# Kernel tuning notes

Hardware: AMD Instinct MI355X
Metric: run time of the kernel (lower is better)

## Reference

```python
import jax, jax.numpy as jnp
import numpy as np

N_ATOMS = 50000   # nAtoms
KMAX = 32         # max neighbors per atom
EMB_ATOM = 256    # emb_size_atom
EMB_PAIR_IN = 64  # emb_size_pair_in
EMB_PAIR_OUT = 64 # emb_size_pair_out
EMB_RBF = 16      # emb_size_rbf
INV_SQRT = lambda n: 1.0 / np.sqrt(n).astype(np.float32)


def setup_inputs() -> dict:
    key = jax.random.key(0)
    k_h, k_rb, k_src, k_wd, k_wb, k_wu = jax.random.split(key, 6)
    h = jax.random.normal(k_h, (N_ATOMS, EMB_ATOM), dtype=jnp.float32)
    rad_basis = jax.random.normal(k_rb, (N_ATOMS, EMB_RBF, KMAX), dtype=jnp.float32)
    # each destination atom has exactly KMAX neighbors -> unique (dst, slot) pairs
    dst = jnp.repeat(jnp.arange(N_ATOMS, dtype=jnp.int64), KMAX)
    src = jax.random.randint(k_src, (N_ATOMS * KMAX,), 0, N_ATOMS, dtype=jnp.int64)
    edge_index = jnp.stack([src, dst])  # (2, nEdges)
    target_neighbor_idx = jnp.tile(jnp.arange(KMAX, dtype=jnp.int64), N_ATOMS)
    W_down = jax.random.normal(k_wd, (EMB_ATOM, EMB_PAIR_IN), dtype=jnp.float32) * INV_SQRT(EMB_ATOM)
    W_bilinear = jax.random.normal(k_wb, (EMB_RBF * EMB_PAIR_IN, EMB_PAIR_OUT), dtype=jnp.float32) * INV_SQRT(EMB_RBF * EMB_PAIR_IN)
    W_up = jax.random.normal(k_wu, (EMB_PAIR_OUT, EMB_ATOM), dtype=jnp.float32) * INV_SQRT(EMB_PAIR_OUT)
    return {"h": h, "rad_basis": rad_basis, "edge_index": edge_index,
            "target_neighbor_idx": target_neighbor_idx,
            "W_down": W_down, "W_bilinear": W_bilinear, "W_up": W_up}


def reference(h, rad_basis, edge_index, target_neighbor_idx, W_down, W_bilinear, W_up):
    num_atoms = h.shape[0]
    kmax = rad_basis.shape[-1]
    # down projection (no bias, no activation)
    x_b = h @ W_down                               # (nAtoms, emb_pair_in)
    x_ba = x_b[edge_index[0]]                      # (nEdges, emb_pair_in) gather from source atoms
    # scatter into dense padded tensor (nAtoms, Kmax, emb_pair_in)
    x2 = jnp.zeros((num_atoms, kmax, x_ba.shape[-1]), dtype=x_ba.dtype)
    x2 = x2.at[edge_index[1], target_neighbor_idx].set(x_ba)
    # per-atom batched matmul with radial basis: (nAtoms, emb_rbf, Kmax) @ (nAtoms, Kmax, emb_pair_in)
    x_ba2 = jnp.einsum('nrk,nkp->nrp', rad_basis, x2)
    # bilinear projection on flattened (emb_rbf * emb_pair_in); ScaleFactor default scale = 1.0 (identity)
    h_out = x_ba2.reshape(num_atoms, -1) @ W_bilinear  # (nAtoms, emb_pair_out)
    return h_out @ W_up                               # (nAtoms, emb_size_atom)
```

## Files before the change

kernel.cpp:

```cpp
#include <hip/hip_runtime.h>

#define N_ATOMS 50000
#define KMAX 32
#define EMB_ATOM 256
#define EP_IN 64
#define EP_OUT 64
#define EMB_RBF 16
#define NEDGES (N_ATOMS * KMAX)

typedef _Float16 half_t;
typedef __attribute__((ext_vector_type(2))) _Float16 half2_t;
typedef __attribute__((ext_vector_type(4))) _Float16 half4_t;
typedef __attribute__((ext_vector_type(8))) _Float16 half8_t;
typedef __attribute__((ext_vector_type(4))) float f32x4;

static_assert(N_ATOMS % 16 == 0, "fused kernel assumes 16 atoms per block");

#define GLOAD_LDS16(g, l)                                                     \
    __builtin_amdgcn_global_load_lds(                                         \
        (const __attribute__((address_space(1))) void*)(g),                   \
        (__attribute__((address_space(3))) void*)(l), 16, 0, 0)

#define XB_NB 782
#define SC_NB (NEDGES / 256)
#define WB_NB 256
#define WU_NB 64
#define PREP_NB (XB_NB + SC_NB + WB_NB + WU_NB + 1)

__global__ __launch_bounds__(256) void prep_all(const float* __restrict__ h,
                                                const float* __restrict__ Wd,
                                                const int*   __restrict__ ei,
                                                const int*   __restrict__ tni,
                                                const float* __restrict__ Wb,
                                                const float* __restrict__ Wu,
                                                half_t* __restrict__ xbh,
                                                int*    __restrict__ sidx,
                                                half_t* __restrict__ Wb2,
                                                half_t* __restrict__ Wu2,
                                                half_t* __restrict__ zrow) {
    __shared__ float As[16 * 68];
    __shared__ float Bs[16 * 64];
    const int bid = blockIdx.x;
    const int t = threadIdx.x;

    if (bid < XB_NB) {
        const int r0 = bid * 64;
        const int tr = t >> 4, tc = t & 15;
        float acc[4][4] = {};
        for (int k0 = 0; k0 < 256; k0 += 16) {
            {
                int m = t >> 2, kk0 = (t & 3) << 2;
                int row = r0 + m;
                float4 v = make_float4(0.f, 0.f, 0.f, 0.f);
                if (row < N_ATOMS)
                    v = *reinterpret_cast<const float4*>(&h[(size_t)row * 256 + k0 + kk0]);
                As[(kk0 + 0) * 68 + m] = v.x;
                As[(kk0 + 1) * 68 + m] = v.y;
                As[(kk0 + 2) * 68 + m] = v.z;
                As[(kk0 + 3) * 68 + m] = v.w;
            }
            {
                int kk = t >> 4, n0 = (t & 15) << 2;
                *reinterpret_cast<float4*>(&Bs[kk * 64 + n0]) =
                    *reinterpret_cast<const float4*>(&Wd[(k0 + kk) * 64 + n0]);
            }
            __syncthreads();
            #pragma unroll
            for (int kk = 0; kk < 16; ++kk) {
                float4 av = *reinterpret_cast<const float4*>(&As[kk * 68 + tr * 4]);
                float4 bv = *reinterpret_cast<const float4*>(&Bs[kk * 64 + tc * 4]);
                float aa[4] = {av.x, av.y, av.z, av.w};
                float bb[4] = {bv.x, bv.y, bv.z, bv.w};
                #pragma unroll
                for (int i = 0; i < 4; ++i)
                    #pragma unroll
                    for (int j = 0; j < 4; ++j) acc[i][j] += aa[i] * bb[j];
            }
            __syncthreads();
        }
        #pragma unroll
        for (int i = 0; i < 4; ++i) {
            int row = r0 + tr * 4 + i;
            if (row < N_ATOMS) {
                half4_t hv;
                #pragma unroll
                for (int j = 0; j < 4; ++j) hv[j] = (half_t)acc[i][j];
                *reinterpret_cast<half4_t*>(&xbh[(size_t)row * 64 + tc * 4]) = hv;
            }
        }
    } else if (bid < XB_NB + SC_NB) {
        int i = (bid - XB_NB) * 256 + t;
        int s = ei[i];
        int d = ei[NEDGES + i];
        int k = tni[i];
        sidx[d * KMAX + k] = s;
    } else if (bid < XB_NB + SC_NB + WB_NB) {
        int i = (bid - XB_NB - SC_NB) * 256 + t;
        int e = i & 7, lv = (i >> 3) & 63;
        int c = lv & 15, g = lv >> 4;
        int kh = (i >> 13) & 1, ot = i >> 14;
        int o = ot * 16 + c;
        int idx = kh * 512 + ((i >> 9) & 15) * 32 + g * 8 + e;
        int r = ((idx >> 6) & 3) * 4 + (idx & 3);
        int p = (idx >> 8) * 16 + ((idx >> 2) & 15);
        Wb2[i] = (half_t)Wb[(size_t)(r * 64 + p) * 64 + o];
    } else if (bid < XB_NB + SC_NB + WB_NB + WU_NB) {
        int i = (bid - XB_NB - SC_NB - WB_NB) * 256 + t;
        int e = i & 7, lv = (i >> 3) & 63;
        int c = lv & 15, g = lv >> 4;
        int kk = (i >> 9) & 1, nt = (i >> 10) & 1, w = i >> 11;
        int oc = w * 32 + nt * 16 + c;
        int o = kk * 32 + g * 8 + e;
        Wu2[i] = (half_t)Wu[(size_t)o * 256 + oc];
    } else {
        if (t < 128) zrow[t] = (half_t)0.f;
    }
}

template <int BUF>
__device__ __forceinline__ void consume_batch(const half_t* stage_h, int c, int g,
                                              half4_t radf, half4_t ident,
                                              f32x4 (&acc)[4]) {
    const f32x4 fzero = {0.f, 0.f, 0.f, 0.f};
    const char* stb = reinterpret_cast<const char*>(stage_h) + BUF * 2048;
    #pragma unroll
    for (int pc = 0; pc < 4; ++pc) {
        int slot = (pc * 2 + (g >> 1)) ^ (c & 7);
        half4_t gf = *reinterpret_cast<const half4_t*>(
            stb + c * 128 + slot * 16 + (g & 1) * 8);
        f32x4 tD = __builtin_amdgcn_mfma_f32_16x16x16f16(gf, ident, fzero, 0, 0, 0);
        half4_t b2;
        #pragma unroll
        for (int j = 0; j < 4; ++j) b2[j] = (half_t)tD[j];
        acc[pc] = __builtin_amdgcn_mfma_f32_16x16x16f16(radf, b2, acc[pc], 0, 0, 0);
    }
}

#define ISSUE(b, buf) do {                                                    \
    { int s_ = sreg[(b) * 2 + 0]; int r_ = (l >> 3);                          \
      const half_t* src_ = ((unsigned)s_ < (unsigned)N_ATOMS)                 \
          ? (xbh + (size_t)s_ * 64) : zrow;                                   \
      src_ += (((l & 7) ^ (r_ & 7)) << 3);                                    \
      GLOAD_LDS16(src_, stage_h + (buf) * 1024); }                            \
    { int s_ = sreg[(b) * 2 + 1]; int r_ = 8 + (l >> 3);                      \
      const half_t* src_ = ((unsigned)s_ < (unsigned)N_ATOMS)                 \
          ? (xbh + (size_t)s_ * 64) : zrow;                                   \
      src_ += (((l & 7) ^ (r_ & 7)) << 3);                                    \
      GLOAD_LDS16(src_, stage_h + (buf) * 1024 + 512); }                      \
} while (0)

#define WAIT_VM(n) do {                                                       \
    asm volatile("s_waitcnt vmcnt(" #n ")" ::: "memory");                     \
    __builtin_amdgcn_sched_barrier(0);                                        \
} while (0)

#define WAIT_LGKM() do {                                                      \
    asm volatile("s_waitcnt lgkmcnt(0)" ::: "memory");                        \
    __builtin_amdgcn_sched_barrier(0);                                        \
} while (0)

__global__ __launch_bounds__(512, 4) void fused(const half_t* __restrict__ xbh,
                                                const float*  __restrict__ rad,
                                                const int*    __restrict__ sidxg,
                                                const half_t* __restrict__ Wb2,
                                                const half_t* __restrict__ Wu2,
                                                const half_t* __restrict__ zrow,
                                                float* __restrict__ out) {
    __shared__ __align__(16) half_t xba2s[16 * 1024];
    __shared__ __align__(16) char   smem_u[32768];

    const int t = threadIdx.x;
    const int w = t >> 6;
    const int l = t & 63;
    const int c = l & 15;
    const int g = l >> 4;
    const int a0 = blockIdx.x * 16;

    float*  preds   = reinterpret_cast<float*>(smem_u);
    half_t* houts   = reinterpret_cast<half_t*>(smem_u + 8704);
    half_t* stage_h = reinterpret_cast<half_t*>(smem_u + (w << 12));

    const f32x4 fzero = {0.f, 0.f, 0.f, 0.f};

    int sreg[4 * 2];
    #pragma unroll
    for (int b = 0; b < 4; ++b)
        #pragma unroll
        for (int hh = 0; hh < 2; ++hh)
            sreg[b * 2 + hh] = sidxg[(size_t)(a0 + w * 2 + (b >> 1)) * KMAX +
                                     (b & 1) * 16 + hh * 8 + (l >> 3)];

    half4_t radF[2][2];
    #pragma unroll
    for (int as = 0; as < 2; ++as) {
        const float* radp = &rad[(size_t)(a0 + w * 2 + as) * 512];
        #pragma unroll
        for (int kc = 0; kc < 2; ++kc) {
            f32x4 rv = *reinterpret_cast<const f32x4*>(radp + c * 32 + kc * 16 + g * 4);
            #pragma unroll
            for (int j = 0; j < 4; ++j) radF[as][kc][j] = (half_t)rv[j];
        }
    }

    half4_t ident;
    #pragma unroll
    for (int j = 0; j < 4; ++j) ident[j] = (half_t)((g * 4 + j == c) ? 1.0f : 0.0f);

    ISSUE(0, 0);
    ISSUE(1, 1);

    f32x4 acc[4] = {fzero, fzero, fzero, fzero};

    WAIT_VM(2);
    consume_batch<0>(stage_h, c, g, radF[0][0], ident, acc);
    WAIT_LGKM();
    ISSUE(2, 0);

    WAIT_VM(2);
    consume_batch<1>(stage_h, c, g, radF[0][1], ident, acc);
    {
        const int a = w * 2;
        #pragma unroll
        for (int pc = 0; pc < 4; ++pc) {
            half4_t hv;
            #pragma unroll
            for (int j = 0; j < 4; ++j) hv[j] = (half_t)acc[pc][j];
            int byte = (a * 2048 + pc * 512 + g * 128 + c * 8) ^ ((a & 7) << 4);
            *reinterpret_cast<half4_t*>(reinterpret_cast<char*>(xba2s) + byte) = hv;
        }
    }
    WAIT_LGKM();
    ISSUE(3, 1);

    #pragma unroll
    for (int pc = 0; pc < 4; ++pc) acc[pc] = fzero;

    WAIT_VM(2);
    consume_batch<0>(stage_h, c, g, radF[1][0], ident, acc);

    WAIT_VM(0);
    consume_batch<1>(stage_h, c, g, radF[1][1], ident, acc);
    {
        const int a = w * 2 + 1;
        #pragma unroll
        for (int pc = 0; pc < 4; ++pc) {
            half4_t hv;
            #pragma unroll
            for (int j = 0; j < 4; ++j) hv[j] = (half_t)acc[pc][j];
            int byte = (a * 2048 + pc * 512 + g * 128 + c * 8) ^ ((a & 7) << 4);
            *reinterpret_cast<half4_t*>(reinterpret_cast<char*>(xba2s) + byte) = hv;
        }
    }

    const int ot = w >> 1, kh = w & 1;
    const half_t* wbbase = &Wb2[(size_t)((ot * 2 + kh) * 16) * 512];
    half8_t bfr[4];
    #pragma unroll
    for (int j = 0; j < 4; ++j)
        bfr[j] = *reinterpret_cast<const half8_t*>(wbbase + j * 512 + l * 8);

    __syncthreads();

    {
        f32x4 acc2[4] = {fzero, fzero, fzero, fzero};
        #pragma unroll
        for (int j = 0; j < 16; ++j) {
            int abyte = (c * 2048 + (kh * 512 + j * 32) * 2 + g * 16) ^ ((c & 7) << 4);
            half8_t af = *reinterpret_cast<const half8_t*>(
                reinterpret_cast<const char*>(xba2s) + abyte);
            half8_t bf = bfr[j & 3];
            if (j + 4 < 16)
                bfr[j & 3] = *reinterpret_cast<const half8_t*>(wbbase + (j + 4) * 512 + l * 8);
            acc2[j & 3] = __builtin_amdgcn_mfma_f32_16x16x32_f16(af, bf, acc2[j & 3], 0, 0, 0);
        }
        f32x4 accT = acc2[0] + acc2[1] + acc2[2] + acc2[3];
        #pragma unroll
        for (int i = 0; i < 4; ++i)
            preds[kh * 1088 + (g * 4 + i) * 68 + ot * 16 + c] = accT[i];
    }

    half8_t wuf[2][2];
    #pragma unroll
    for (int nt = 0; nt < 2; ++nt)
        #pragma unroll
        for (int kk = 0; kk < 2; ++kk)
            wuf[nt][kk] = *reinterpret_cast<const half8_t*>(
                &Wu2[(size_t)(((w * 2 + nt) * 2 + kk) * 64 + l) * 8]);

    __syncthreads();

    {
        int m = t >> 5, oj = (t & 31) << 1;
        float s0 = preds[m * 68 + oj]     + preds[1088 + m * 68 + oj];
        float s1 = preds[m * 68 + oj + 1] + preds[1088 + m * 68 + oj + 1];
        half2_t hv; hv[0] = (half_t)s0; hv[1] = (half_t)s1;
        int byte = (m * 128 + oj * 2) ^ ((m & 7) << 4);
        *reinterpret_cast<half2_t*>(reinterpret_cast<char*>(houts) + byte) = hv;
    }
    __syncthreads();

    half8_t ha[2];
    #pragma unroll
    for (int kk = 0; kk < 2; ++kk) {
        int byte = (c * 128 + kk * 64 + g * 16) ^ ((c & 7) << 4);
        ha[kk] = *reinterpret_cast<const half8_t*>(
            reinterpret_cast<const char*>(houts) + byte);
    }
    #pragma unroll
    for (int nt = 0; nt < 2; ++nt) {
        int oc0 = w * 32 + nt * 16;
        f32x4 acc3 = fzero;
        #pragma unroll
        for (int kk = 0; kk < 2; ++kk)
            acc3 = __builtin_amdgcn_mfma_f32_16x16x32_f16(ha[kk], wuf[nt][kk], acc3, 0, 0, 0);
        #pragma unroll
        for (int i = 0; i < 4; ++i)
            out[(size_t)(a0 + g * 4 + i) * 256 + oc0 + c] = acc3[i];
    }
}

extern "C" void kernel_launch(void* const* d_in, const int* in_sizes, int n_in,
                              void* d_out, int out_size, void* d_ws, size_t ws_size,
                              hipStream_t stream) {
    const float* h   = (const float*)d_in[0];
    const float* rad = (const float*)d_in[1];
    const int*   ei  = (const int*)d_in[2];
    const int*   tni = (const int*)d_in[3];
    const float* Wd  = (const float*)d_in[4];
    const float* Wb  = (const float*)d_in[5];
    const float* Wu  = (const float*)d_in[6];
    float* out = (float*)d_out;

    half_t* xbh  = (half_t*)d_ws;
    int*    sidx = (int*)((char*)d_ws + (size_t)N_ATOMS * EP_IN * sizeof(half_t));
    half_t* Wb2  = (half_t*)((char*)sidx + (size_t)NEDGES * sizeof(int));
    half_t* Wu2  = Wb2 + 64 * 1024;
    half_t* zrow = Wu2 + 16384;

    prep_all<<<PREP_NB, 256, 0, stream>>>(h, Wd, ei, tni, Wb, Wu,
                                          xbh, sidx, Wb2, Wu2, zrow);
    fused<<<N_ATOMS / 16, 512, 0, stream>>>(xbh, rad, sidx, Wb2, Wu2, zrow, out);
}
```

Baseline: 88.26 us.

## Reuse xba2s region as gather staging to cut LDS and raise occupancy

The per-wave gather staging buffers now live inside the xba2s LDS region that each wave later overwrites with its own results, and the separate 32KB union buffer is replaced by small preds/houts arrays. This lowers LDS per block so more blocks fit per CU, and the launch bound goes from 4 to 6 waves-per-EU. Source indices are loaded once per lane and redistributed with shuffles, and radial-basis values are loaded coalesced and then shuffled into MFMA fragment order. Weight loads are issued earlier to overlap with the gathers. The risks are register pressure under the tighter bound and correctness hazards from aliasing staging with result storage.

After: 85.41 us. 3.2% less time.

```diff
diff --git a/kernel.cpp b/kernel.cpp
--- a/kernel.cpp
+++ b/kernel.cpp
@@ -117,12 +117,10 @@
     }
 }
 
-template <int BUF>
-__device__ __forceinline__ void consume_batch(const half_t* stage_h, int c, int g,
+__device__ __forceinline__ void consume_batch(const char* stb, int c, int g,
                                               half4_t radf, half4_t ident,
                                               f32x4 (&acc)[4]) {
     const f32x4 fzero = {0.f, 0.f, 0.f, 0.f};
-    const char* stb = reinterpret_cast<const char*>(stage_h) + BUF * 2048;
     #pragma unroll
     for (int pc = 0; pc < 4; ++pc) {
         int slot = (pc * 2 + (g >> 1)) ^ (c & 7);
@@ -136,17 +134,27 @@
     }
 }
 
-#define ISSUE(b, buf) do {                                                    \
-    { int s_ = sreg[(b) * 2 + 0]; int r_ = (l >> 3);                          \
-      const half_t* src_ = ((unsigned)s_ < (unsigned)N_ATOMS)                 \
-          ? (xbh + (size_t)s_ * 64) : zrow;                                   \
-      src_ += (((l & 7) ^ (r_ & 7)) << 3);                                    \
-      GLOAD_LDS16(src_, stage_h + (buf) * 1024); }                            \
-    { int s_ = sreg[(b) * 2 + 1]; int r_ = 8 + (l >> 3);                      \
-      const half_t* src_ = ((unsigned)s_ < (unsigned)N_ATOMS)                 \
-          ? (xbh + (size_t)s_ * 64) : zrow;                                   \
-      src_ += (((l & 7) ^ (r_ & 7)) << 3);                                    \
-      GLOAD_LDS16(src_, stage_h + (buf) * 1024 + 512); }                      \
+#define ISSUE(as, kc, bufb) do {                                              \
+    _Pragma("unroll")                                                         \
+    for (int h_ = 0; h_ < 2; ++h_) {                                          \
+        int s_ = __shfl(sv, (as) * 32 + (kc) * 16 + h_ * 8 + (l >> 3), 64);   \
+        const half_t* src_ = ((unsigned)s_ < (unsigned)N_ATOMS)               \
+            ? (xbh + (size_t)s_ * 64) : zrow;                                 \
+        src_ += (((l & 7) ^ (l >> 3)) << 3);          \
+        GLOAD_LDS16(src_, (half_t*)(Rbase + (bufb)) + h_ * 512);              \
+    }                                                                         \
+} while (0)
+
+#define WRITE_ATOM(a_, accv) do {                                             \
+    _Pragma("unroll")                                                         \
+    for (int pc = 0; pc < 4; ++pc) {                                          \
+        half4_t hv;                                                           \
+        _Pragma("unroll")                                                     \
+        for (int j = 0; j < 4; ++j) hv[j] = (half_t)accv[pc][j];              \
+        int byte_ = ((a_) * 2048 + pc * 512 + g * 128 + c * 8) ^              \
+                    (((a_) & 7) << 4);                                        \
+        *reinterpret_cast<half4_t*>(reinterpret_cast<char*>(xba2s) + byte_) = hv; \
+    }                                                                         \
 } while (0)
 
 #define WAIT_VM(n) do {                                                       \
@@ -159,7 +167,7 @@
     __builtin_amdgcn_sched_barrier(0);                                        \
 } while (0)
 
-__global__ __launch_bounds__(512, 4) void fused(const half_t* __restrict__ xbh,
+__global__ __launch_bounds__(512, 6) void fused(const half_t* __restrict__ xbh,
                                                 const float*  __restrict__ rad,
                                                 const int*    __restrict__ sidxg,
                                                 const half_t* __restrict__ Wb2,
@@ -167,7 +175,8 @@
                                                 const half_t* __restrict__ zrow,
                                                 float* __restrict__ out) {
     __shared__ __align__(16) half_t xba2s[16 * 1024];
-    __shared__ __align__(16) char   smem_u[32768];
+    __shared__ __align__(16) float  preds[2 * 16 * 68];
+    __shared__ __align__(16) half_t houts[16 * 64];
 
     const int t = threadIdx.x;
     const int w = t >> 6;
@@ -176,81 +185,20 @@
     const int g = l >> 4;
     const int a0 = blockIdx.x * 16;
 
-    float*  preds   = reinterpret_cast<float*>(smem_u);
-    half_t* houts   = reinterpret_cast<half_t*>(smem_u + 8704);
-    half_t* stage_h = reinterpret_cast<half_t*>(smem_u + (w << 12));
+    char* Rbase = reinterpret_cast<char*>(xba2s) + w * 4096;
 
     const f32x4 fzero = {0.f, 0.f, 0.f, 0.f};
 
-    int sreg[4 * 2];
-    #pragma unroll
-    for (int b = 0; b < 4; ++b)
-        #pragma unroll
-        for (int hh = 0; hh < 2; ++hh)
-            sreg[b * 2 + hh] = sidxg[(size_t)(a0 + w * 2 + (b >> 1)) * KMAX +
-                                     (b & 1) * 16 + hh * 8 + (l >> 3)];
-
-    half4_t radF[2][2];
-    #pragma unroll
-    for (int as = 0; as < 2; ++as) {
-        const float* radp = &rad[(size_t)(a0 + w * 2 + as) * 512];
-        #pragma unroll
-        for (int kc = 0; kc < 2; ++kc) {
-            f32x4 rv = *reinterpret_cast<const f32x4*>(radp + c * 32 + kc * 16 + g * 4);
-            #pragma unroll
-            for (int j = 0; j < 4; ++j) radF[as][kc][j] = (half_t)rv[j];
-        }
-    }
-
-    half4_t ident;
-    #pragma unroll
-    for (int j = 0; j < 4; ++j) ident[j] = (half_t)((g * 4 + j == c) ? 1.0f : 0.0f);
-
-    ISSUE(0, 0);
-    ISSUE(1, 1);
-
-    f32x4 acc[4] = {fzero, fzero, fzero, fzero};
-
-    WAIT_VM(2);
-    consume_batch<0>(stage_h, c, g, radF[0][0], ident, acc);
-    WAIT_LGKM();
-    ISSUE(2, 0);
-
-    WAIT_VM(2);
-    consume_batch<1>(stage_h, c, g, radF[0][1], ident, acc);
-    {
-        const int a = w * 2;
-        #pragma unroll
-        for (int pc = 0; pc < 4; ++pc) {
-            half4_t hv;
-            #pragma unroll
-            for (int j = 0; j < 4; ++j) hv[j] = (half_t)acc[pc][j];
-            int byte = (a * 2048 + pc * 512 + g * 128 + c * 8) ^ ((a & 7) << 4);
-            *reinterpret_cast<half4_t*>(reinterpret_cast<char*>(xba2s) + byte) = hv;
-        }
-    }
-    WAIT_LGKM();
-    ISSUE(3, 1);
-
-    #pragma unroll
-    for (int pc = 0; pc < 4; ++pc) acc[pc] = fzero;
-
-    WAIT_VM(2);
-    consume_batch<0>(stage_h, c, g, radF[1][0], ident, acc);
-
-    WAIT_VM(0);
-    consume_batch<1>(stage_h, c, g, radF[1][1], ident, acc);
-    {
-        const int a = w * 2 + 1;
-        #pragma unroll
-        for (int pc = 0; pc < 4; ++pc) {
-            half4_t hv;
-            #pragma unroll
-            for (int j = 0; j < 4; ++j) hv[j] = (half_t)acc[pc][j];
-            int byte = (a * 2048 + pc * 512 + g * 128 + c * 8) ^ ((a & 7) << 4);
-            *reinterpret_cast<half4_t*>(reinterpret_cast<char*>(xba2s) + byte) = hv;
-        }
-    }
+    int sv = sidxg[(size_t)(a0 + w * 2) * KMAX + l];
+    const float* radw = &rad[(size_t)(a0 + w * 2) * 512];
+    f32x4 rv[4];
+    #pragma unroll
+    for (int q = 0; q < 4; ++q)
+        rv[q] = *reinterpret_cast<const f32x4*>(radw + q * 256 + l * 4);
+
+    ISSUE(0, 0, 0);
+    ISSUE(0, 1, 2048);
+    __builtin_amdgcn_sched_barrier(0);
 
     const int ot = w >> 1, kh = w & 1;
     const half_t* wbbase = &Wb2[(size_t)((ot * 2 + kh) * 16) * 512];
@@ -258,6 +206,43 @@
     #pragma unroll
     for (int j = 0; j < 4; ++j)
         bfr[j] = *reinterpret_cast<const half8_t*>(wbbase + j * 512 + l * 8);
+    __builtin_amdgcn_sched_barrier(0);
+
+    half4_t radF[2][2];
+    #pragma unroll
+    for (int as = 0; as < 2; ++as)
+        #pragma unroll
+        for (int kc = 0; kc < 2; ++kc) {
+            int srcl = (c & 7) * 8 + kc * 4 + g;
+            #pragma unroll
+            for (int j = 0; j < 4; ++j) {
+                float lo = __shfl(rv[as * 2 + 0][j], srcl, 64);
+                float hi = __shfl(rv[as * 2 + 1][j], srcl, 64);
+                radF[as][kc][j] = (half_t)((c & 8) ? hi : lo);
+            }
+        }
+
+    half4_t ident;
+    #pragma unroll
+    for (int j = 0; j < 4; ++j) ident[j] = (half_t)((g * 4 + j == c) ? 1.0f : 0.0f);
+
+    f32x4 acc0[4] = {fzero, fzero, fzero, fzero};
+    f32x4 acc1[4] = {fzero, fzero, fzero, fzero};
+
+    WAIT_VM(6);
+    consume_batch(Rbase, c, g, radF[0][0], ident, acc0);
+    WAIT_LGKM();
+    ISSUE(1, 0, 0);
+    WAIT_VM(6);
+    consume_batch(Rbase + 2048, c, g, radF[0][1], ident, acc0);
+    WAIT_LGKM();
+    ISSUE(1, 1, 2048);
+    WAIT_VM(2);
+    consume_batch(Rbase, c, g, radF[1][0], ident, acc1);
+    WRITE_ATOM(w * 2, acc0);
+    WAIT_VM(0);
+    consume_batch(Rbase + 2048, c, g, radF[1][1], ident, acc1);
+    WRITE_ATOM(w * 2 + 1, acc1);
 
     __syncthreads();
 
@@ -294,17 +279,17 @@
         float s0 = preds[m * 68 + oj]     + preds[1088 + m * 68 + oj];
         float s1 = preds[m * 68 + oj + 1] + preds[1088 + m * 68 + oj + 1];
         half2_t hv; hv[0] = (half_t)s0; hv[1] = (half_t)s1;
-        int byte = (m * 128 + oj * 2) ^ ((m & 7) << 4);
-        *reinterpret_cast<half2_t*>(reinterpret_cast<char*>(houts) + byte) = hv;
+        int byte_ = (m * 128 + oj * 2) ^ ((m & 7) << 4);
+        *reinterpret_cast<half2_t*>(reinterpret_cast<char*>(houts) + byte_) = hv;
     }
     __syncthreads();
 
     half8_t ha[2];
     #pragma unroll
     for (int kk = 0; kk < 2; ++kk) {
-        int byte = (c * 128 + kk * 64 + g * 16) ^ ((c & 7) << 4);
+        int byte_ = (c * 128 + kk * 64 + g * 16) ^ ((c & 7) << 4);
         ha[kk] = *reinterpret_cast<const half8_t*>(
-            reinterpret_cast<const char*>(houts) + byte);
+            reinterpret_cast<const char*>(houts) + byte_);
     }
     #pragma unroll
     for (int nt = 0; nt < 2; ++nt) {
```
